# Kernel optimization log

Measured on AMD Instinct MI355X. Metric: run time of the kernel, lower is better.

Reference implementation:

```python
import jax, jax.numpy as jnp
import numpy as np

B, S, D, H = 2, 2048, 1024, 16
HD = D // H  # head_dim = 64
ROPE_BASE = 10000.0


def apply_rope(x, positions):
    # x: [B, S, H, HD], positions: [B, S] int. Rotate-half RoPE.
    d = x.shape[-1]
    inv_freq = 1.0 / (ROPE_BASE ** (jnp.arange(0, d, 2, dtype=jnp.float32) / d))  # [d/2]
    ang = positions[..., None].astype(jnp.float32) * inv_freq  # [B, S, d/2]
    cos = jnp.cos(ang)[:, :, None, :]
    sin = jnp.sin(ang)[:, :, None, :]
    x1, x2 = jnp.split(x, 2, axis=-1)
    return jnp.concatenate([x1 * cos - x2 * sin, x2 * cos + x1 * sin], axis=-1).astype(x.dtype)


def setup_inputs() -> dict:
    key = jax.random.key(0)
    k1, k2, k3 = jax.random.split(key, 3)
    inputs = jax.random.normal(k1, (B, S, D), dtype=jnp.float32)
    # nn.Linear weights [out_features, in_features]
    W_in = jax.random.normal(k2, (3 * D, D), dtype=jnp.float32) * (1.0 / np.sqrt(D))
    W_out = jax.random.normal(k3, (D, D), dtype=jnp.float32) * (1.0 / np.sqrt(D))
    positions = jnp.tile(jnp.arange(S, dtype=jnp.int32)[None, :], (B, 1))  # [B, S]
    return {"inputs": inputs, "positions": positions, "W_in": W_in, "W_out": W_out}


def reference(inputs, positions, W_in, W_out):
    # fused QKV projection: [B, S, 3D], head-major layout per rearrange '(heads qkv)'
    qkv = jnp.einsum('bsd,ed->bse', inputs, W_in)
    qkv = qkv.reshape(B, S, H, 3 * HD)
    q, k, v = jnp.split(qkv, 3, axis=-1)  # each [B, S, H, HD]
    q = apply_rope(q, positions)
    k = apply_rope(k, positions)
    # einsum_attention (inference path): scale query, full masked softmax
    q = q / jnp.sqrt(jnp.asarray(HD, dtype=q.dtype))
    scores = jnp.einsum('bqhd,bkhd->bhqk', q, k)  # [B, H, S, S]
    mask = (jnp.arange(S)[None, None, :] <= positions[:, :, None])[:, None, :, :]  # [B,1,S,S]
    big_neg = jnp.finfo(scores.dtype).min
    scores = jnp.where(mask, scores, big_neg)
    attn = jax.nn.softmax(scores, axis=-1)
    x = jnp.einsum('bhqk,bkhd->bqhd', attn, v).reshape(B, S, D)
    return jnp.einsum('bsd,ed->bse', x, W_out)
```

## Files before the change

kernel.cpp:

```cpp
#include <hip/hip_runtime.h>
#include <stdint.h>
#include <math.h>

#define B_ 2
#define S_ 2048
#define D_ 1024
#define H_ 16
#define HD_ 64
#define KVBLK 64

typedef __bf16 bf16_t;
typedef __bf16 bf16x4 __attribute__((ext_vector_type(4)));
typedef __bf16 bf16x8 __attribute__((ext_vector_type(8)));
typedef float f32x4 __attribute__((ext_vector_type(4)));
typedef float f32x16 __attribute__((ext_vector_type(16)));
typedef float float4v __attribute__((ext_vector_type(4)));

#define L2E 1.4426950408889634f
#define NINF (-__builtin_inff())

__device__ __forceinline__ void gload_lds16(const bf16_t* g, bf16_t* l) {
  __builtin_amdgcn_global_load_lds((const __attribute__((address_space(1))) void*)g,
                                   (__attribute__((address_space(3))) void*)l, 16, 0, 0);
}

__device__ __forceinline__ uint32_t packbf(float a, float b) {
  union { __bf16 h[2]; uint32_t u; } cvt;
  cvt.h[0] = (__bf16)a; cvt.h[1] = (__bf16)b;
  return cvt.u;
}

__global__ void cast3_bf16_kernel(const float* __restrict__ s0, bf16_t* __restrict__ d0, int n0,
                                  const float* __restrict__ s1, bf16_t* __restrict__ d1, int n1,
                                  const float* __restrict__ s2, bf16_t* __restrict__ d2, int n2) {
  int i = blockIdx.x * blockDim.x + threadIdx.x;
  int stride = gridDim.x * blockDim.x;
  int tot = n0 + n1 + n2;
  for (; i < tot; i += stride) {
    const float* s; bf16_t* d; int j = i;
    if (j < n0) { s = s0; d = d0; }
    else if ((j -= n0) < n1) { s = s1; d = d1; }
    else { j -= n1; s = s2; d = d2; }
    float4v f = *(const float4v*)(s + (size_t)j * 4);
    bf16x4 o;
    o[0] = (__bf16)f[0]; o[1] = (__bf16)f[1]; o[2] = (__bf16)f[2]; o[3] = (__bf16)f[3];
    *(bf16x4*)(d + (size_t)j * 4) = o;
  }
}

template <typename OutT>
__global__ __launch_bounds__(256) void gemm_bt(const bf16_t* __restrict__ A,
                                               const bf16_t* __restrict__ Bm,
                                               OutT* __restrict__ C,
                                               int M, int N, int K) {
  __shared__ bf16_t As[128 * 32];
  __shared__ bf16_t Bs[128 * 32];
  const int t = threadIdx.x;
  const int lane = t & 63, wave = t >> 6;
  const int wr = wave >> 1, wc = wave & 1;
  const int qr = lane & 15, g = lane >> 4;
  const int bm = blockIdx.x, bn = blockIdx.y;

  f32x4 acc[4][4];
#pragma unroll
  for (int m = 0; m < 4; m++)
#pragma unroll
    for (int n = 0; n < 4; n++) acc[m][n] = (f32x4){0.f, 0.f, 0.f, 0.f};

  const bf16_t* Abase = A + (size_t)(bm * 128) * K;
  const bf16_t* Bbase = Bm + (size_t)(bn * 128) * K;
  const int srow = t >> 2;
  const int scol = (t & 3) * 8;

  for (int kk = 0; kk < K; kk += 32) {
    gload_lds16(Abase + (size_t)srow * K + kk + scol,        As + t * 8);
    gload_lds16(Abase + (size_t)(srow + 64) * K + kk + scol, As + 2048 + t * 8);
    gload_lds16(Bbase + (size_t)srow * K + kk + scol,        Bs + t * 8);
    gload_lds16(Bbase + (size_t)(srow + 64) * K + kk + scol, Bs + 2048 + t * 8);
    __syncthreads();
    bf16x8 a[4], b[4];
#pragma unroll
    for (int m = 0; m < 4; m++)
      a[m] = *(const bf16x8*)(As + (wr * 64 + m * 16 + qr) * 32 + g * 8);
#pragma unroll
    for (int n = 0; n < 4; n++)
      b[n] = *(const bf16x8*)(Bs + (wc * 64 + n * 16 + qr) * 32 + g * 8);
#pragma unroll
    for (int m = 0; m < 4; m++)
#pragma unroll
      for (int n = 0; n < 4; n++)
        acc[m][n] = __builtin_amdgcn_mfma_f32_16x16x32_bf16(a[m], b[n], acc[m][n], 0, 0, 0);
    __syncthreads();
  }

#pragma unroll
  for (int m = 0; m < 4; m++) {
    int row0 = bm * 128 + wr * 64 + m * 16 + g * 4;
#pragma unroll
    for (int n = 0; n < 4; n++) {
      int col = bn * 128 + wc * 64 + n * 16 + qr;
#pragma unroll
      for (int r = 0; r < 4; r++)
        C[(size_t)(row0 + r) * N + col] = (OutT)acc[m][n][r];
    }
  }
}

__global__ __launch_bounds__(512, 1) void gemm_qkv_rope(const bf16_t* __restrict__ A,
                                                        const bf16_t* __restrict__ Bm,
                                                        const int* __restrict__ pos,
                                                        bf16_t* __restrict__ Qd,
                                                        bf16_t* __restrict__ Kd,
                                                        bf16_t* __restrict__ Vtd) {
  const int K = D_;
  const int NT = K >> 6;
  __shared__ bf16_t As[2][256 * 64];
  __shared__ bf16_t Bs[2][256 * 64];
  const int t = threadIdx.x;
  const int lane = t & 63, wid = t >> 6;
  const int qr = lane & 15, g = lane >> 4;
  const int wm = wid >> 2, wn = wid & 3;
  const int bm = blockIdx.x, bn = blockIdx.y;

  const bf16_t* Ab = A + (size_t)(bm * 256) * K;
  const bf16_t* Bb = Bm + (size_t)(bn * 256) * K;

  const bf16_t* srcA[4];
  const bf16_t* srcB[4];
  int ldsOff[4];
#pragma unroll
  for (int i = 0; i < 4; i++) {
    int e = t + 512 * i;
    int row = e >> 3, cs = e & 7;
    int gcol = (cs ^ (row & 7)) * 8;
    srcA[i] = Ab + (size_t)row * K + gcol;
    srcB[i] = Bb + (size_t)row * K + gcol;
    ldsOff[i] = e * 8;
  }

  f32x4 acc[8][4];
#pragma unroll
  for (int m = 0; m < 8; m++)
#pragma unroll
    for (int n = 0; n < 4; n++) acc[m][n] = (f32x4){0.f, 0.f, 0.f, 0.f};

#define RD(buf_, r_, k_) (*(const bf16x8*)((buf_) + (r_) * 64 + ((((k_) * 4 + g) ^ ((r_) & 7)) * 8)))

#pragma unroll
  for (int i = 0; i < 4; i++) gload_lds16(srcA[i], As[0] + ldsOff[i]);
#pragma unroll
  for (int i = 0; i < 4; i++) gload_lds16(srcB[i], Bs[0] + ldsOff[i]);
#pragma unroll
  for (int i = 0; i < 4; i++) gload_lds16(srcA[i] + 64, As[1] + ldsOff[i]);
#pragma unroll
  for (int i = 0; i < 4; i++) gload_lds16(srcB[i] + 64, Bs[1] + ldsOff[i]);

  for (int T = 0; T < NT; ++T) {
    bf16_t* A_c = As[T & 1];
    bf16_t* B_c = Bs[T & 1];
    if (T + 1 < NT) asm volatile("s_waitcnt vmcnt(8)" ::: "memory");
    else            asm volatile("s_waitcnt vmcnt(0)" ::: "memory");
    __builtin_amdgcn_sched_barrier(0);
    __builtin_amdgcn_s_barrier();

    const bool st = (T + 2 < NT);
    const int kt2 = (T + 2) * 64;

    bf16x8 alo[4][2], ahi[4][2], bfr[4][2];

#pragma unroll
    for (int m = 0; m < 4; m++) {
      int r = wm * 128 + m * 16 + qr;
      alo[m][0] = RD(A_c, r, 0); alo[m][1] = RD(A_c, r, 1);
    }
#pragma unroll
    for (int n = 0; n < 2; n++) {
      int r = wn * 64 + n * 16 + qr;
      bfr[n][0] = RD(B_c, r, 0); bfr[n][1] = RD(B_c, r, 1);
    }
    __builtin_amdgcn_s_barrier();
    __builtin_amdgcn_s_setprio(1);
#pragma unroll
    for (int m = 0; m < 4; m++)
#pragma unroll
      for (int n = 0; n < 2; n++)
#pragma unroll
        for (int k = 0; k < 2; k++)
          acc[m][n] = __builtin_amdgcn_mfma_f32_16x16x32_bf16(alo[m][k], bfr[n][k], acc[m][n], 0, 0, 0);
    __builtin_amdgcn_s_setprio(0);
    __builtin_amdgcn_s_barrier();

#pragma unroll
    for (int n = 2; n < 4; n++) {
      int r = wn * 64 + n * 16 + qr;
      bfr[n][0] = RD(B_c, r, 0); bfr[n][1] = RD(B_c, r, 1);
    }
    if (st) {
      gload_lds16(srcA[0] + kt2, A_c + ldsOff[0]);
      gload_lds16(srcA[2] + kt2, A_c + ldsOff[2]);
    }
    __builtin_amdgcn_s_barrier();
    __builtin_amdgcn_s_setprio(1);
#pragma unroll
    for (int m = 0; m < 4; m++)
#pragma unroll
      for (int n = 2; n < 4; n++)
#pragma unroll
        for (int k = 0; k < 2; k++)
          acc[m][n] = __builtin_amdgcn_mfma_f32_16x16x32_bf16(alo[m][k], bfr[n][k], acc[m][n], 0, 0, 0);
    __builtin_amdgcn_s_setprio(0);
    __builtin_amdgcn_s_barrier();

#pragma unroll
    for (int m = 0; m < 4; m++) {
      int r = wm * 128 + (m + 4) * 16 + qr;
      ahi[m][0] = RD(A_c, r, 0); ahi[m][1] = RD(A_c, r, 1);
    }
    if (st) {
      gload_lds16(srcB[0] + kt2, B_c + ldsOff[0]);
      gload_lds16(srcB[1] + kt2, B_c + ldsOff[1]);
      gload_lds16(srcB[2] + kt2, B_c + ldsOff[2]);
      gload_lds16(srcB[3] + kt2, B_c + ldsOff[3]);
    }
    __builtin_amdgcn_s_barrier();
    __builtin_amdgcn_s_setprio(1);
#pragma unroll
    for (int m = 0; m < 4; m++)
#pragma unroll
      for (int n = 0; n < 2; n++)
#pragma unroll
        for (int k = 0; k < 2; k++)
          acc[m + 4][n] = __builtin_amdgcn_mfma_f32_16x16x32_bf16(ahi[m][k], bfr[n][k], acc[m + 4][n], 0, 0, 0);
    __builtin_amdgcn_s_setprio(0);
    __builtin_amdgcn_s_barrier();

    if (st) {
      gload_lds16(srcA[1] + kt2, A_c + ldsOff[1]);
      gload_lds16(srcA[3] + kt2, A_c + ldsOff[3]);
    }
    __builtin_amdgcn_s_barrier();
    __builtin_amdgcn_s_setprio(1);
#pragma unroll
    for (int m = 0; m < 4; m++)
#pragma unroll
      for (int n = 2; n < 4; n++)
#pragma unroll
        for (int k = 0; k < 2; k++)
          acc[m + 4][n] = __builtin_amdgcn_mfma_f32_16x16x32_bf16(ahi[m][k], bfr[n][k], acc[m + 4][n], 0, 0, 0);
    __builtin_amdgcn_s_setprio(0);
    __builtin_amdgcn_s_barrier();
  }
#undef RD

  __syncthreads();
  bf16_t* myLds = (wid < 4) ? ((bf16_t*)As + wid * 8192) : ((bf16_t*)Bs + (wid - 4) * 8192);

  const int w = bn * 4 + wn;
  const int typ = w % 3;
  const int head = w / 3;
  const int rowbase = bm * 256 + wm * 128;
  const int b = rowbase >> 11;
  const int s0w = rowbase & (S_ - 1);

  if (typ == 2) {
#pragma unroll
    for (int m = 0; m < 8; m++) {
      int sl0 = m * 16 + g * 4;
#pragma unroll
      for (int n = 0; n < 4; n++) {
        int d = n * 16 + qr;
#pragma unroll
        for (int rr = 0; rr < 4; rr++) {
          int sl = sl0 + rr;
          myLds[d * 128 + (((sl >> 3) ^ (d & 15)) * 8) + (sl & 7)] = (__bf16)acc[m][n][rr];
        }
      }
    }
    bf16_t* dstv = Vtd + (size_t)(b * H_ + head) * HD_ * S_ + s0w;
#pragma unroll
    for (int it = 0; it < 16; it++) {
      int d = (lane >> 4) + it * 4;
      int sc = lane & 15;
      bf16x8 v = *(const bf16x8*)(myLds + d * 128 + ((sc ^ (d & 15)) * 8));
      *(bf16x8*)(dstv + (size_t)d * S_ + sc * 8) = v;
    }
  } else {
    const float qs = (typ == 0) ? 0.125f : 1.0f;
    const float l2r = 13.287712379549449f / 32.0f;
    float inv[2];
    inv[0] = exp2f(-(float)qr * l2r);
    inv[1] = exp2f(-(float)(qr + 16) * l2r);
#pragma unroll
    for (int m = 0; m < 8; m++) {
      int r0 = m * 16 + g * 4;
#pragma unroll
      for (int rr = 0; rr < 4; rr++) {
        int r = r0 + rr;
        float p = (float)pos[rowbase + r];
#pragma unroll
        for (int n = 0; n < 2; n++) {
          float ang = p * inv[n];
          float sn = __sinf(ang);
          float cs = __cosf(ang);
          float x1 = acc[m][n][rr], x2 = acc[m][n + 2][rr];
          float o1 = (x1 * cs - x2 * sn) * qs;
          float o2 = (x2 * cs + x1 * sn) * qs;
          int d1 = n * 16 + qr, d2 = d1 + 32;
          myLds[r * 64 + (((d1 >> 3) ^ (r & 7)) * 8) + (d1 & 7)] = (__bf16)o1;
          myLds[r * 64 + (((d2 >> 3) ^ (r & 7)) * 8) + (d2 & 7)] = (__bf16)o2;
        }
      }
    }
    bf16_t* dstb = ((typ == 0) ? Qd : Kd) + (size_t)(b * H_ + head) * S_ * HD_ + (size_t)s0w * HD_;
#pragma unroll
    for (int it = 0; it < 16; it++) {
      int r = (lane >> 3) + it * 8;
      int cc = lane & 7;
      bf16x8 v = *(const bf16x8*)(myLds + r * 64 + ((cc ^ (r & 7)) * 8));
      *(bf16x8*)(dstb + (size_t)r * HD_ + cc * 8) = v;
    }
  }
}

__global__ __launch_bounds__(256) void attn_kernel(const bf16_t* __restrict__ Q,
                                                   const bf16_t* __restrict__ K,
                                                   const bf16_t* __restrict__ Vt,
                                                   const int* __restrict__ pos,
                                                   bf16_t* __restrict__ O,
                                                   bf16_t* __restrict__ Opart,
                                                   float* __restrict__ Mst,
                                                   float* __restrict__ Lst) {
  __shared__ bf16_t Ks[2][64 * 64];
  __shared__ bf16_t Vs[2][64 * 64];

  const int t = threadIdx.x;
  const int lane = t & 63, wv = t >> 6;
  const int l31 = lane & 31, hi = lane >> 5;

  const int bid = blockIdx.x;
  const int bh = (bid & 7) * 4 + ((bid >> 3) & 3);
  const int v5 = bid >> 5;
  const int qblk = 15 - (v5 >> 1);
  const int half = v5 & 1;
  const int b = bh >> 4, h = bh & 15;
  const int q0 = qblk * 128;

  const bf16_t* Qb = Q + (size_t)bh * (S_ * HD_);
  const bf16_t* Kb = K + (size_t)bh * (S_ * HD_);
  const bf16_t* Vb = Vt + (size_t)bh * (HD_ * S_);

  const int qrow = q0 + wv * 32 + l31;

  const int prow = pos[b * S_ + qrow];
  int wmin = prow;
#pragma unroll
  for (int off = 1; off < 32; off <<= 1) wmin = min(wmin, __shfl_xor(wmin, off));

  int mp = max(pos[b * S_ + q0 + lane], pos[b * S_ + q0 + 64 + lane]);
#pragma unroll
  for (int off = 1; off < 64; off <<= 1) mp = max(mp, __shfl_xor(mp, off));
  const int nt = min(S_ / KVBLK, (mp >> 6) + 1);

  const int t0 = half * 16;
  const int t1 = min(nt, t0 + 16);
  if (t0 >= t1) return;
  const bool needs_merge = (nt > 16);

  bf16x8 qf[4];
#pragma unroll
  for (int c = 0; c < 4; c++)
    qf[c] = *(const bf16x8*)(Qb + (size_t)qrow * HD_ + c * 16 + hi * 8);

  const int r0 = t >> 3, c0 = t & 7;
  const int r1 = (t + 256) >> 3, c1 = t & 7;
  const bf16_t* KgA = Kb + (size_t)r0 * HD_ + ((c0 ^ (r0 & 7)) * 8);
  const bf16_t* KgB = Kb + (size_t)r1 * HD_ + ((c1 ^ (r1 & 7)) * 8);
  const bf16_t* VgA = Vb + (size_t)r0 * S_ + ((c0 ^ (r0 & 7)) * 8);
  const bf16_t* VgB = Vb + (size_t)r1 * S_ + ((c1 ^ (r1 & 7)) * 8);
  const int ldsA = t * 8, ldsB = (t + 256) * 8;

  f32x16 oT[2];
#pragma unroll
  for (int dt = 0; dt < 2; dt++)
#pragma unroll
    for (int r = 0; r < 16; r++) oT[dt][r] = 0.f;
  float m_run = NINF, l_run = 0.f;

  {
    const int kn = t0 * KVBLK;
    gload_lds16(KgA + (size_t)kn * HD_, Ks[0] + ldsA);
    gload_lds16(KgB + (size_t)kn * HD_, Ks[0] + ldsB);
    gload_lds16(VgA + kn, Vs[0] + ldsA);
    gload_lds16(VgB + kn, Vs[0] + ldsB);
  }
  __syncthreads();

  for (int kt = t0; kt < t1; ++kt) {
    const int k0 = kt * KVBLK;
    const int cur = kt & 1;
    if (kt + 1 < t1) {
      const int kn = (kt + 1) * KVBLK;
      gload_lds16(KgA + (size_t)kn * HD_, Ks[cur ^ 1] + ldsA);
      gload_lds16(KgB + (size_t)kn * HD_, Ks[cur ^ 1] + ldsB);
      gload_lds16(VgA + kn, Vs[cur ^ 1] + ldsA);
      gload_lds16(VgB + kn, Vs[cur ^ 1] + ldsB);
    }
    const bf16_t* Kc = Ks[cur];
    const bf16_t* Vc = Vs[cur];

    f32x16 s0, s1;
#pragma unroll
    for (int r = 0; r < 16; r++) { s0[r] = 0.f; s1[r] = 0.f; }
    __builtin_amdgcn_s_setprio(1);
#pragma unroll
    for (int c = 0; c < 4; c++) {
      const int c2 = c * 2 + hi;
      const int kr0 = l31;
      const int kr1 = 32 + l31;
      bf16x8 kf0 = *(const bf16x8*)(Kc + kr0 * 64 + ((c2 ^ (kr0 & 7)) * 8));
      bf16x8 kf1 = *(const bf16x8*)(Kc + kr1 * 64 + ((c2 ^ (kr1 & 7)) * 8));
      s0 = __builtin_amdgcn_mfma_f32_32x32x16_bf16(kf0, qf[c], s0, 0, 0, 0);
      s1 = __builtin_amdgcn_mfma_f32_32x32x16_bf16(kf1, qf[c], s1, 0, 0, 0);
    }
    __builtin_amdgcn_s_setprio(0);

    float p0[16], p1[16];
    if (k0 + 63 > wmin) {
#pragma unroll
      for (int r = 0; r < 16; r++) {
        int koff = (r & 3) + 8 * (r >> 2) + 4 * hi;
        p0[r] = (k0 + koff <= prow) ? s0[r] : NINF;
        p1[r] = (k0 + 32 + koff <= prow) ? s1[r] : NINF;
      }
    } else {
#pragma unroll
      for (int r = 0; r < 16; r++) { p0[r] = s0[r]; p1[r] = s1[r]; }
    }

    float tm = NINF;
#pragma unroll
    for (int r = 0; r < 16; r++) tm = fmaxf(tm, fmaxf(p0[r], p1[r]));
    tm = fmaxf(tm, __shfl_xor(tm, 32));
    if (__any(tm > m_run + 8.0f)) {
      float mn = fmaxf(fmaxf(m_run, tm), -1e30f);
      float scale = exp2f((m_run - mn) * L2E);
      l_run *= scale;
#pragma unroll
      for (int dt = 0; dt < 2; dt++)
#pragma unroll
        for (int r = 0; r < 16; r++) oT[dt][r] *= scale;
      m_run = mn;
    }
    const float mnl = (m_run == NINF) ? 3.0e38f : m_run * L2E;
    float rs = 0.f;
#pragma unroll
    for (int r = 0; r < 16; r++) {
      p0[r] = exp2f(p0[r] * L2E - mnl);
      p1[r] = exp2f(p1[r] * L2E - mnl);
      rs += p0[r] + p1[r];
    }
    rs += __shfl_xor(rs, 32);
    l_run += rs;

#pragma unroll
    for (int kc = 0; kc < 4; kc++) {
      const float* P = (kc < 2) ? p0 : p1;
      const int rb = (kc & 1) * 8;
      uint32_t xa0 = packbf(P[rb + 0], P[rb + 1]);
      uint32_t xa1 = packbf(P[rb + 2], P[rb + 3]);
      uint32_t xb0 = packbf(P[rb + 4], P[rb + 5]);
      uint32_t xb1 = packbf(P[rb + 6], P[rb + 7]);
      uint32_t sa0 = (uint32_t)__shfl_xor((int)xa0, 32);
      uint32_t sa1 = (uint32_t)__shfl_xor((int)xa1, 32);
      uint32_t sb0 = (uint32_t)__shfl_xor((int)xb0, 32);
      uint32_t sb1 = (uint32_t)__shfl_xor((int)xb1, 32);
      union { uint32_t u[4]; bf16x8 v; } pf;
      pf.u[0] = hi ? sb0 : xa0;
      pf.u[1] = hi ? sb1 : xa1;
      pf.u[2] = hi ? xb0 : sa0;
      pf.u[3] = hi ? xb1 : sa1;
      __builtin_amdgcn_s_setprio(1);
#pragma unroll
      for (int dt = 0; dt < 2; dt++) {
        const int vr = dt * 32 + l31;
        const int c2 = kc * 2 + hi;
        bf16x8 vf = *(const bf16x8*)(Vc + vr * 64 + ((c2 ^ (vr & 7)) * 8));
        oT[dt] = __builtin_amdgcn_mfma_f32_32x32x16_bf16(vf, pf.v, oT[dt], 0, 0, 0);
      }
      __builtin_amdgcn_s_setprio(0);
    }

    __syncthreads();
  }

  const float rl = needs_merge ? 1.0f : ((l_run > 0.f) ? 1.0f / l_run : 0.f);
  bf16_t* Ot = (bf16_t*)Ks + wv * 2048;
#pragma unroll
  for (int dt = 0; dt < 2; dt++)
#pragma unroll
    for (int r = 0; r < 16; r++) {
      int chunk = dt * 4 + (r >> 2);
      int el = (r & 3) + 4 * hi;
      Ot[l31 * 64 + ((chunk ^ (l31 & 7)) * 8) + el] = (__bf16)(oT[dt][r] * rl);
    }
  __syncthreads();
  if (needs_merge) {
    bf16_t* dst = Opart + (((size_t)(half * 32 + bh) * 16 + qblk) * 128) * 64;
#pragma unroll
    for (int it = 0; it < 4; it++) {
      int qr2 = (lane >> 3) + it * 8;
      int cc = lane & 7;
      bf16x8 vv = *(const bf16x8*)(Ot + qr2 * 64 + ((cc ^ (qr2 & 7)) * 8));
      *(bf16x8*)(&dst[(size_t)(wv * 32 + qr2) * 64 + cc * 8]) = vv;
    }
    if (hi == 0) {
      size_t sidx = ((size_t)(half * 32 + bh) * 16 + qblk) * 128 + wv * 32 + l31;
      Mst[sidx] = m_run;
      Lst[sidx] = l_run;
    }
  } else {
#pragma unroll
    for (int it = 0; it < 4; it++) {
      int qr2 = (lane >> 3) + it * 8;
      int cc = lane & 7;
      bf16x8 vv = *(const bf16x8*)(Ot + qr2 * 64 + ((cc ^ (qr2 & 7)) * 8));
      *(bf16x8*)(&O[(size_t)(b * S_ + q0 + wv * 32 + qr2) * D_ + h * 64 + cc * 8]) = vv;
    }
  }
}

__global__ __launch_bounds__(256) void attn_merge_kernel(const bf16_t* __restrict__ Opart,
                                                         const float* __restrict__ Mst,
                                                         const float* __restrict__ Lst,
                                                         const int* __restrict__ pos,
                                                         bf16_t* __restrict__ O) {
  __shared__ int wmax_s[4];
  const int t = threadIdx.x;
  const int bid = blockIdx.x;
  const int bh = (bid & 7) * 4 + ((bid >> 3) & 3);
  const int qblk = 15 - (bid >> 5);
  const int b = bh >> 4, h = bh & 15;
  const int q0 = qblk * 128;

  int p = pos[b * S_ + q0 + (t & 127)];
#pragma unroll
  for (int off = 1; off < 64; off <<= 1) p = max(p, __shfl_xor(p, off));
  if ((t & 63) == 0) wmax_s[t >> 6] = p;
  __syncthreads();
  int mp = max(max(wmax_s[0], wmax_s[1]), max(wmax_s[2], wmax_s[3]));
  if ((mp >> 6) + 1 <= 16) return;

  const int r = t >> 1, dh = (t & 1) * 32;
  const size_t s0i = ((size_t)(0 * 32 + bh) * 16 + qblk) * 128 + r;
  const size_t s1i = ((size_t)(1 * 32 + bh) * 16 + qblk) * 128 + r;
  float m0 = Mst[s0i], l0 = Lst[s0i];
  float m1 = Mst[s1i], l1 = Lst[s1i];
  float m = fmaxf(fmaxf(m0, m1), -1e30f);
  float w0 = exp2f((m0 - m) * L2E);
  float w1 = exp2f((m1 - m) * L2E);
  float lt = l0 * w0 + l1 * w1;
  float rl = (lt > 0.f) ? 1.0f / lt : 0.f;
  w0 *= rl; w1 *= rl;
  const bf16_t* pa = Opart + s0i * 64 + dh;
  const bf16_t* pb = Opart + s1i * 64 + dh;
  bf16_t* dst = O + (size_t)(b * S_ + q0 + r) * D_ + h * 64 + dh;
#pragma unroll
  for (int c = 0; c < 4; c++) {
    bf16x8 a = *(const bf16x8*)(pa + c * 8);
    bf16x8 bb = *(const bf16x8*)(pb + c * 8);
    bf16x8 o;
#pragma unroll
    for (int j = 0; j < 8; j++)
      o[j] = (__bf16)((float)a[j] * w0 + (float)bb[j] * w1);
    *(bf16x8*)(dst + c * 8) = o;
  }
}

extern "C" void kernel_launch(void* const* d_in, const int* in_sizes, int n_in,
                              void* d_out, int out_size, void* d_ws, size_t ws_size,
                              hipStream_t stream) {
  const float* inputs = (const float*)d_in[0];
  const int* positions = (const int*)d_in[1];
  const float* W_in = (const float*)d_in[2];
  const float* W_out = (const float*)d_in[3];
  float* out = (float*)d_out;

  bf16_t* X_bf = (bf16_t*)d_ws;
  bf16_t* Win_bf = X_bf + (size_t)4096 * 1024;
  bf16_t* Wout_bf = Win_bf + (size_t)3072 * 1024;
  bf16_t* scratch = Wout_bf + (size_t)1024 * 1024;
  bf16_t* Qb = scratch + (size_t)4096 * 3072;
  bf16_t* Kb = Qb + (size_t)B_ * H_ * S_ * HD_;
  bf16_t* Vtb = Kb + (size_t)B_ * H_ * S_ * HD_;
  bf16_t* Ob = Vtb + (size_t)B_ * H_ * S_ * HD_;

  bf16_t* Opart = scratch;
  float* Mst = (float*)(scratch + (size_t)2 * 32 * 16 * 128 * 64);
  float* Lst = Mst + (size_t)2 * 32 * 16 * 128;

  cast3_bf16_kernel<<<dim3(2048), dim3(256), 0, stream>>>(
      inputs, X_bf, (4096 * 1024) / 4,
      W_in, Win_bf, (3072 * 1024) / 4,
      W_out, Wout_bf, (1024 * 1024) / 4);

  gemm_qkv_rope<<<dim3(16, 12), dim3(512), 0, stream>>>(X_bf, Win_bf, positions, Qb, Kb, Vtb);

  attn_kernel<<<dim3(1024), dim3(256), 0, stream>>>(Qb, Kb, Vtb, positions, Ob, Opart, Mst, Lst);
  attn_merge_kernel<<<dim3(512), dim3(256), 0, stream>>>(Opart, Mst, Lst, positions, Ob);

  gemm_bt<float><<<dim3(32, 8), dim3(256), 0, stream>>>(Ob, Wout_bf, out, 4096, 1024, 1024);
}
```

Measured before the change: 147.6 us.

## Split attention KV range into four chunks with multi-way merge

Splits each query block's KV range into up to four chunks of 8 tiles instead of two halves of 16, doubling the attention grid. The merge kernel now combines up to four partial results using the running max and sum statistics. Workspace is reused by aliasing the partial outputs and statistics onto the bf16 input and weight buffers, which are dead by that point. The aim is better load balance across CUs for the causal triangle, at the cost of more partial-output traffic and merge work.

```diff
diff --git a/kernel.cpp b/kernel.cpp
--- a/kernel.cpp
+++ b/kernel.cpp
@@ -8,6 +8,8 @@
 #define H_ 16
 #define HD_ 64
 #define KVBLK 64
+#define CHTILES 8
+#define CHELEMS ((size_t)32 * 16 * 128 * 64)
 
 typedef __bf16 bf16_t;
 typedef __bf16 bf16x4 __attribute__((ext_vector_type(4)));
@@ -327,7 +329,8 @@
                                                    const bf16_t* __restrict__ Vt,
                                                    const int* __restrict__ pos,
                                                    bf16_t* __restrict__ O,
-                                                   bf16_t* __restrict__ Opart,
+                                                   bf16_t* __restrict__ Op0,
+                                                   bf16_t* __restrict__ Op3,
                                                    float* __restrict__ Mst,
                                                    float* __restrict__ Lst) {
   __shared__ bf16_t Ks[2][64 * 64];
@@ -339,9 +342,9 @@
 
   const int bid = blockIdx.x;
   const int bh = (bid & 7) * 4 + ((bid >> 3) & 3);
-  const int v5 = bid >> 5;
-  const int qblk = 15 - (v5 >> 1);
-  const int half = v5 & 1;
+  const int v6 = bid >> 5;
+  const int qblk = 15 - (v6 >> 2);
+  const int chunk = v6 & 3;
   const int b = bh >> 4, h = bh & 15;
   const int q0 = qblk * 128;
 
@@ -361,10 +364,10 @@
   for (int off = 1; off < 64; off <<= 1) mp = max(mp, __shfl_xor(mp, off));
   const int nt = min(S_ / KVBLK, (mp >> 6) + 1);
 
-  const int t0 = half * 16;
-  const int t1 = min(nt, t0 + 16);
+  const int t0 = chunk * CHTILES;
+  const int t1 = min(nt, t0 + CHTILES);
   if (t0 >= t1) return;
-  const bool needs_merge = (nt > 16);
+  const bool needs_merge = (nt > CHTILES);
 
   bf16x8 qf[4];
 #pragma unroll
@@ -499,13 +502,14 @@
   for (int dt = 0; dt < 2; dt++)
 #pragma unroll
     for (int r = 0; r < 16; r++) {
-      int chunk = dt * 4 + (r >> 2);
+      int chunkq = dt * 4 + (r >> 2);
       int el = (r & 3) + 4 * hi;
-      Ot[l31 * 64 + ((chunk ^ (l31 & 7)) * 8) + el] = (__bf16)(oT[dt][r] * rl);
+      Ot[l31 * 64 + ((chunkq ^ (l31 & 7)) * 8) + el] = (__bf16)(oT[dt][r] * rl);
     }
   __syncthreads();
   if (needs_merge) {
-    bf16_t* dst = Opart + (((size_t)(half * 32 + bh) * 16 + qblk) * 128) * 64;
+    bf16_t* dst = ((chunk < 3) ? (Op0 + (size_t)chunk * CHELEMS) : Op3)
+                + ((size_t)(bh * 16 + qblk) * 128) * 64;
 #pragma unroll
     for (int it = 0; it < 4; it++) {
       int qr2 = (lane >> 3) + it * 8;
@@ -514,7 +518,7 @@
       *(bf16x8*)(&dst[(size_t)(wv * 32 + qr2) * 64 + cc * 8]) = vv;
     }
     if (hi == 0) {
-      size_t sidx = ((size_t)(half * 32 + bh) * 16 + qblk) * 128 + wv * 32 + l31;
+      size_t sidx = ((size_t)(chunk * 32 + bh) * 16 + qblk) * 128 + wv * 32 + l31;
       Mst[sidx] = m_run;
       Lst[sidx] = l_run;
     }
@@ -529,7 +533,8 @@
   }
 }
 
-__global__ __launch_bounds__(256) void attn_merge_kernel(const bf16_t* __restrict__ Opart,
+__global__ __launch_bounds__(256) void attn_merge_kernel(const bf16_t* __restrict__ Op0,
+                                                         const bf16_t* __restrict__ Op3,
                                                          const float* __restrict__ Mst,
                                                          const float* __restrict__ Lst,
                                                          const int* __restrict__ pos,
@@ -548,31 +553,44 @@
   if ((t & 63) == 0) wmax_s[t >> 6] = p;
   __syncthreads();
   int mp = max(max(wmax_s[0], wmax_s[1]), max(wmax_s[2], wmax_s[3]));
-  if ((mp >> 6) + 1 <= 16) return;
+  const int nt = min(S_ / KVBLK, (mp >> 6) + 1);
+  const int nch = (nt + CHTILES - 1) / CHTILES;
+  if (nch <= 1) return;
 
   const int r = t >> 1, dh = (t & 1) * 32;
-  const size_t s0i = ((size_t)(0 * 32 + bh) * 16 + qblk) * 128 + r;
-  const size_t s1i = ((size_t)(1 * 32 + bh) * 16 + qblk) * 128 + r;
-  float m0 = Mst[s0i], l0 = Lst[s0i];
-  float m1 = Mst[s1i], l1 = Lst[s1i];
-  float m = fmaxf(fmaxf(m0, m1), -1e30f);
-  float w0 = exp2f((m0 - m) * L2E);
-  float w1 = exp2f((m1 - m) * L2E);
-  float lt = l0 * w0 + l1 * w1;
-  float rl = (lt > 0.f) ? 1.0f / lt : 0.f;
-  w0 *= rl; w1 *= rl;
-  const bf16_t* pa = Opart + s0i * 64 + dh;
-  const bf16_t* pb = Opart + s1i * 64 + dh;
+  const size_t rowoff = ((size_t)(bh * 16 + qblk) * 128 + r) * 64 + dh;
+
+  float mc[4], lc[4];
+  float m = -1e30f;
+  for (int c = 0; c < nch; c++) {
+    size_t sidx = ((size_t)(c * 32 + bh) * 16 + qblk) * 128 + r;
+    mc[c] = Mst[sidx];
+    lc[c] = Lst[sidx];
+    m = fmaxf(m, mc[c]);
+  }
+  float accv[32];
+#pragma unroll
+  for (int j = 0; j < 32; j++) accv[j] = 0.f;
+  float lt = 0.f;
+  for (int c = 0; c < nch; c++) {
+    float wgt = exp2f((mc[c] - m) * L2E);
+    lt += lc[c] * wgt;
+    const bf16_t* pc = ((c < 3) ? (Op0 + (size_t)c * CHELEMS) : Op3) + rowoff;
+#pragma unroll
+    for (int cc4 = 0; cc4 < 4; cc4++) {
+      bf16x8 v = *(const bf16x8*)(pc + cc4 * 8);
+#pragma unroll
+      for (int j = 0; j < 8; j++) accv[cc4 * 8 + j] += wgt * (float)v[j];
+    }
+  }
+  const float rl = (lt > 0.f) ? 1.0f / lt : 0.f;
   bf16_t* dst = O + (size_t)(b * S_ + q0 + r) * D_ + h * 64 + dh;
 #pragma unroll
-  for (int c = 0; c < 4; c++) {
-    bf16x8 a = *(const bf16x8*)(pa + c * 8);
-    bf16x8 bb = *(const bf16x8*)(pb + c * 8);
+  for (int cc4 = 0; cc4 < 4; cc4++) {
     bf16x8 o;
 #pragma unroll
-    for (int j = 0; j < 8; j++)
-      o[j] = (__bf16)((float)a[j] * w0 + (float)bb[j] * w1);
-    *(bf16x8*)(dst + c * 8) = o;
+    for (int j = 0; j < 8; j++) o[j] = (__bf16)(accv[cc4 * 8 + j] * rl);
+    *(bf16x8*)(dst + cc4 * 8) = o;
   }
 }
 
@@ -594,9 +612,10 @@
   bf16_t* Vtb = Kb + (size_t)B_ * H_ * S_ * HD_;
   bf16_t* Ob = Vtb + (size_t)B_ * H_ * S_ * HD_;
 
-  bf16_t* Opart = scratch;
-  float* Mst = (float*)(scratch + (size_t)2 * 32 * 16 * 128 * 64);
-  float* Lst = Mst + (size_t)2 * 32 * 16 * 128;
+  bf16_t* Op0 = scratch;
+  bf16_t* Op3 = X_bf;
+  float* Mst = (float*)Win_bf;
+  float* Lst = Mst + (size_t)4 * 32 * 16 * 128;
 
   cast3_bf16_kernel<<<dim3(2048), dim3(256), 0, stream>>>(
       inputs, X_bf, (4096 * 1024) / 4,
@@ -605,8 +624,8 @@
 
   gemm_qkv_rope<<<dim3(16, 12), dim3(512), 0, stream>>>(X_bf, Win_bf, positions, Qb, Kb, Vtb);
 
-  attn_kernel<<<dim3(1024), dim3(256), 0, stream>>>(Qb, Kb, Vtb, positions, Ob, Opart, Mst, Lst);
-  attn_merge_kernel<<<dim3(512), dim3(256), 0, stream>>>(Opart, Mst, Lst, positions, Ob);
+  attn_kernel<<<dim3(2048), dim3(256), 0, stream>>>(Qb, Kb, Vtb, positions, Ob, Op0, Op3, Mst, Lst);
+  attn_merge_kernel<<<dim3(512), dim3(256), 0, stream>>>(Op0, Op3, Mst, Lst, positions, Ob);
 
   gemm_bt<float><<<dim3(32, 8), dim3(256), 0, stream>>>(Ob, Wout_bf, out, 4096, 1024, 1024);
 }
```

Result: faster. 141.4 us (-4.2%).
